# Kernel optimization log

Measured on AMD Instinct MI355X. Metric: run time of the kernel, lower is better.

Reference implementation:

```python
import jax, jax.numpy as jnp
import numpy as np
from jax import lax

# PRPN constants (match init_kwargs)
NSLOTS = 15
NLOOKBACK = 1
RESOLUTION = 0.1
NLAYERS = 2
H = 1024      # nhid == ninp
NTOKEN = 32000
T, B = 256, 64
INF = 1e8


def masked_softmax(x, mask):
    # PRPN blocks.softmax: exp-normalize then multiply by gate mask
    e = jnp.exp(x - jnp.max(x, axis=-1, keepdims=True))
    e = e * mask
    return e / (jnp.sum(e, axis=-1, keepdims=True) + 1e-8)


def setup_inputs() -> dict:
    key = jax.random.key(0)
    ks = jax.random.split(key, 16)
    s = 0.02
    return {
        'tokens': jax.random.randint(ks[0], (T, B), 0, NTOKEN),
        'emb_table': s * jax.random.normal(ks[1], (NTOKEN, H), jnp.float32),
        'conv1_w': s * jax.random.normal(ks[2], (H, H, NLOOKBACK + 1), jnp.float32),
        'conv1_b': jnp.zeros((H,), jnp.float32),
        'bn1_gamma': jnp.ones((H,), jnp.float32),
        'bn1_beta': jnp.zeros((H,), jnp.float32),
        'conv2_w': s * jax.random.normal(ks[3], (2, H // 2, 1), jnp.float32),
        'conv2_b': jnp.zeros((2,), jnp.float32),
        'reader_wih': s * jax.random.normal(ks[4], (NLAYERS, 4 * H, H), jnp.float32),
        'reader_whh': s * jax.random.normal(ks[5], (NLAYERS, 4 * H, H), jnp.float32),
        'reader_bih': jnp.zeros((NLAYERS, 4 * H), jnp.float32),
        'reader_bhh': jnp.zeros((NLAYERS, 4 * H), jnp.float32),
        'reader_summ_w': s * jax.random.normal(ks[6], (NLAYERS, H, 2 * H), jnp.float32),
        'reader_summ_b': jnp.zeros((NLAYERS, H), jnp.float32),
        'pred_summ_w': s * jax.random.normal(ks[7], (H, 2 * H), jnp.float32),
        'pred_summ_b': jnp.zeros((H,), jnp.float32),
        'ffd_w': s * jax.random.normal(ks[8], (H, 2 * H), jnp.float32),
        'ffd_b': jnp.zeros((H,), jnp.float32),
        'ffd_gamma': jnp.ones((H,), jnp.float32),
        'ffd_beta': jnp.zeros((H,), jnp.float32),
    }


def _parser_gates(emb, conv1_w, conv1_b, bn1_gamma, bn1_beta, conv2_w, conv2_b):
    # emb: (T, B, H). Parser state init: zeros lookback embs, +inf cum_gate.
    t = emb.shape[0]
    emb_last = jnp.concatenate([jnp.zeros((NLOOKBACK,) + emb.shape[1:], emb.dtype), emb], axis=0)
    x = jnp.transpose(emb_last, (1, 2, 0))  # (B, H, T+lookback)
    h = lax.conv_general_dilated(x, conv1_w, (1,), 'VALID',
                                 dimension_numbers=('NCH', 'OIH', 'NCH'))
    h = h + conv1_b[None, :, None]
    h = bn1_gamma[None, :, None] * h + bn1_beta[None, :, None]  # BatchNorm1d (eval, mean=0,var=1)
    h = jax.nn.relu(h)
    g = lax.conv_general_dilated(h, conv2_w, (1,), 'VALID', feature_group_count=2,
                                 dimension_numbers=('NCH', 'OIH', 'NCH'))
    g = jax.nn.sigmoid(g + conv2_b[None, :, None])  # (B, 2, T)
    gate, gate_next = g[:, 0], g[:, 1]  # (B, T)
    cum_gate = jnp.concatenate([jnp.full((gate.shape[0], NSLOTS), INF, gate.dtype), gate], axis=1)
    # gate_hat[:, t, j] = cum_gate[:, (NSLOTS - j) + t], slots stacked for i = NSLOTS..1
    idx = jnp.arange(t)[:, None] + (NSLOTS - jnp.arange(NSLOTS))[None, :]
    gate_hat = cum_gate[:, idx]  # (B, T, NSLOTS)
    mg = jnp.cumprod(jax.nn.sigmoid((gate[:, :, None] - gate_hat) / RESOLUTION * 10 + 5), axis=2)
    mgn = jnp.cumprod(jax.nn.sigmoid((gate_next[:, :, None] - gate_hat) / RESOLUTION * 10 + 5), axis=2)
    return mg, mgn  # (B, T, NSLOTS)


def _prpn_forward(tokens, emb_table, conv1_w, conv1_b, bn1_gamma, bn1_beta, conv2_w, conv2_b,
                  reader_wih, reader_whh, reader_bih, reader_bhh, reader_summ_w, reader_summ_b,
                  pred_summ_w, pred_summ_b, ffd_w, ffd_b, ffd_gamma, ffd_beta):
    t, b = tokens.shape
    emb = emb_table[tokens]  # (T, B, H)
    mg, mgn = _parser_gates(emb, conv1_w, conv1_b, bn1_gamma, bn1_beta, conv2_w, conv2_b)
    mg_t = jnp.transpose(mg, (1, 0, 2))   # (T, B, S)
    mgn_t = jnp.transpose(mgn, (1, 0, 2))
    inv_sqrt_h = 1.0 / np.sqrt(H).astype(np.float32)

    def step(carry, xs):
        rh, rc, pm = carry  # (L,B,S,H), (L,B,S,H), (B,S,H)
        emb_i, mg_i, mgn_i = xs
        h = emb_i
        new_rh, new_rc = [], []
        for j in range(NLAYERS):
            mh, mc = rh[j], rc[j]
            key = jnp.concatenate([h, mh[:, -1]], axis=1) @ reader_summ_w[j].T + reader_summ_b[j]
            logits = jnp.einsum('bsh,bh->bs', mh, key) * inv_sqrt_h
            att = masked_softmax(logits, mg_i)
            sel_h = jnp.einsum('bs,bsh->bh', att, mh)
            sel_c = jnp.einsum('bs,bsh->bh', att, mc)
            gates = h @ reader_wih[j].T + reader_bih[j] + sel_h @ reader_whh[j].T + reader_bhh[j]
            ig, fg, gg, og = jnp.split(gates, 4, axis=1)
            c_new = jax.nn.sigmoid(fg) * sel_c + jax.nn.sigmoid(ig) * jnp.tanh(gg)
            h = jax.nn.sigmoid(og) * jnp.tanh(c_new)
            new_rh.append(jnp.concatenate([mh[:, 1:], h[:, None]], axis=1))
            new_rc.append(jnp.concatenate([mc[:, 1:], c_new[:, None]], axis=1))
        # predictor attention over its own slot memory, gated by memory_gate_next
        key = jnp.concatenate([h, pm[:, -1]], axis=1) @ pred_summ_w.T + pred_summ_b
        logits = jnp.einsum('bsh,bh->bs', pm, key) * inv_sqrt_h
        att = masked_softmax(logits, mgn_i)
        sel = jnp.einsum('bs,bsh->bh', att, pm)
        pm = jnp.concatenate([pm[:, 1:], h[:, None]], axis=1)
        return (jnp.stack(new_rh), jnp.stack(new_rc), pm), (h, sel)

    z = jnp.zeros((NLAYERS, b, NSLOTS, H), emb.dtype)
    carry0 = (z, z, jnp.zeros((b, NSLOTS, H), emb.dtype))
    _, (hs, sels) = lax.scan(step, carry0, (emb, mg_t, mgn_t))
    x = jnp.concatenate([hs.reshape(-1, H), sels.reshape(-1, H)], axis=1)  # (T*B, 2H)
    out = jnp.tanh(ffd_gamma * (x @ ffd_w.T + ffd_b) + ffd_beta)  # PredictNetwork.ffd (BN eval)
    return out


def reference(tokens, emb_table, conv1_w, conv1_b, bn1_gamma, bn1_beta, conv2_w, conv2_b,
              reader_wih, reader_whh, reader_bih, reader_bhh, reader_summ_w, reader_summ_b,
              pred_summ_w, pred_summ_b, ffd_w, ffd_b, ffd_gamma, ffd_beta):
    out = _prpn_forward(tokens, emb_table, conv1_w, conv1_b, bn1_gamma, bn1_beta, conv2_w, conv2_b,
                        reader_wih, reader_whh, reader_bih, reader_bhh, reader_summ_w, reader_summ_b,
                        pred_summ_w, pred_summ_b, ffd_w, ffd_b, ffd_gamma, ffd_beta)
    mask = tokens != 0
    return out, mask
```

## Files before the change

kernel.cpp:

```cpp
#include <hip/hip_runtime.h>


typedef _Float16 half8 __attribute__((ext_vector_type(8)));
typedef float f32x4 __attribute__((ext_vector_type(4)));

#define LSTR 56

__device__ __forceinline__ float sigm(float x) { return 1.0f / (1.0f + expf(-x)); }

__device__ __forceinline__ void store_ct(float* p, float v)    { *p = v; }
__device__ __forceinline__ void store_ct(_Float16* p, float v) { *p = (_Float16)v; }

__device__ __forceinline__ void mfma_loop(const _Float16* __restrict__ Ag, int lda,
                                          const _Float16* __restrict__ Bg, int ldb,
                                          int K, _Float16* As, _Float16* Bs, f32x4* acc)
{
  const int tid = threadIdx.x;
  const int lr  = tid >> 2;
  const int lc  = (tid & 3) << 3;
  const int ln  = tid & 63;
  const int wv  = tid >> 6;
  const int m15 = ln & 15;
  const int q   = ln >> 4;
  const _Float16* ap = Ag + (size_t)lr * lda + lc;
  const _Float16* bp = Bg + (size_t)lr * ldb + lc;
  _Float16* asw = As + lr * LSTR + lc;
  _Float16* bsw = Bs + lr * LSTR + lc;
  const _Float16* asr = As + (wv * 16 + m15) * LSTR + q * 8;
  const _Float16* bsr = Bs + m15 * LSTR + q * 8;
  half8 av = *(const half8*)ap;
  half8 bv = *(const half8*)bp;
  for (int k0 = 0; k0 < K; k0 += 32) {
    __syncthreads();
    *(half8*)asw = av;
    *(half8*)bsw = bv;
    __syncthreads();
    if (k0 + 32 < K) {
      ap += 32; bp += 32;
      av = *(const half8*)ap;
      bv = *(const half8*)bp;
    }
    half8 a = *(const half8*)asr;
#pragma unroll
    for (int j = 0; j < 4; j++) {
      half8 b = *(const half8*)(bsr + j * 16 * LSTR);
      acc[j] = __builtin_amdgcn_mfma_f32_16x16x32_f16(a, b, acc[j], 0, 0, 0);
    }
  }
}

template <int ACT, typename CT>
__global__ __launch_bounds__(256) void gemm_bt(const _Float16* __restrict__ A, int lda,
                                               const _Float16* __restrict__ B, int ldb,
                                               CT* __restrict__ C, int ldc, int K,
                                               const float* __restrict__ p0,
                                               const float* __restrict__ p1,
                                               const float* __restrict__ p2)
{
  __shared__ __align__(16) _Float16 As[64 * LSTR];
  __shared__ __align__(16) _Float16 Bs[64 * LSTR];
  f32x4 acc[4] = {};
  const int ntile = blockIdx.x, mtile = blockIdx.y;
  mfma_loop(A + (size_t)mtile * 64 * lda, lda, B + (size_t)ntile * 64 * ldb, ldb, K, As, Bs, acc);
  const int ln = threadIdx.x & 63, wv = threadIdx.x >> 6;
  const int m15 = ln & 15, q = ln >> 4;
#pragma unroll
  for (int j = 0; j < 4; j++) {
    const int col = ntile * 64 + j * 16 + m15;
    float b0 = 0.f, b1 = 0.f, b2 = 0.f;
    if (ACT == 0) {
      if (p0) b0 = p0[col];
      if (p1) b0 += p1[col];
    } else {
      b0 = p0[col]; b1 = p1[col]; b2 = p2[col];
    }
#pragma unroll
    for (int r = 0; r < 4; r++) {
      const int row = mtile * 64 + wv * 16 + q * 4 + r;
      float v = acc[j][r];
      if (ACT == 0) v += b0;
      else {
        v = b0 * (v + b1) + b2;
        v = (ACT == 1) ? fmaxf(v, 0.f) : tanhf(v);
      }
      store_ct(&C[(size_t)row * ldc + col], v);
    }
  }
}

struct SegP { const _Float16* B; float* C; const float* b1; const float* b2; int ldb; int ldc; };

__device__ void bundle_tile(const _Float16* __restrict__ A, const SegP sg, int ntile,
                            _Float16* As, _Float16* Bs)
{
  f32x4 acc[4] = {};
  mfma_loop(A, 1024, sg.B + (size_t)ntile * 64 * sg.ldb, sg.ldb, 1024, As, Bs, acc);
  const int ln = threadIdx.x & 63, wv = threadIdx.x >> 6;
  const int m15 = ln & 15, q = ln >> 4;
#pragma unroll
  for (int j = 0; j < 4; j++) {
    const int col = ntile * 64 + j * 16 + m15;
    float bb = 0.f;
    if (sg.b1) bb += sg.b1[col];
    if (sg.b2) bb += sg.b2[col];
#pragma unroll
    for (int r = 0; r < 4; r++) {
      const int row = wv * 16 + q * 4 + r;
      sg.C[(size_t)row * sg.ldc + col] = acc[j][r] + bb;
    }
  }
}

template <typename KT, typename GT>
__device__ void cell_body(int b, int c0, int nch, int t,
    const KT* __restrict__ keyA, const float* __restrict__ keyB,
    const GT* __restrict__ gatesIn,
    const float* __restrict__ ringH, const float* __restrict__ ringC,
    const float* __restrict__ proj, const float* __restrict__ mask,
    float* __restrict__ hRingOut, float* __restrict__ cRingOut,
    _Float16* __restrict__ hHalf, float* s_key, float* s_att)
{
  const int tid = threadIdx.x;
  for (int i = tid; i < 1024; i += 256)
    s_key[i] = (float)keyA[b * 1024 + i] + keyB[b * 1024 + i];
  __syncthreads();
  const int wv = tid >> 6, ln = tid & 63;
  for (int s = wv; s < 15; s += 4) {
    const float* hr = ringH + ((size_t)((t + s) & 15) * 64 + b) * 1024;
    float p = 0.f;
    for (int i = ln; i < 1024; i += 64) p = fmaf(hr[i], s_key[i], p);
    for (int off = 32; off > 0; off >>= 1) p += __shfl_down(p, off, 64);
    if (ln == 0) s_att[s] = p * 0.03125f;
  }
  __syncthreads();
  if (tid == 0) {
    float mx = -1e30f;
    for (int s = 0; s < 15; s++) mx = fmaxf(mx, s_att[s]);
    float den = 1e-8f, e[15];
    for (int s = 0; s < 15; s++) { e[s] = expf(s_att[s] - mx) * mask[b * 15 + s]; den += e[s]; }
    float inv = 1.f / den;
    for (int s = 0; s < 15; s++) s_att[s] = e[s] * inv;
  }
  __syncthreads();
  float att[15];
  int poff[15], coff[15];
#pragma unroll
  for (int s = 0; s < 15; s++) {
    att[s] = s_att[s];
    const int phs = (t + s) & 15;
    poff[s] = phs * 262144 + b * 4096;
    coff[s] = phs * 65536 + b * 1024;
  }
  for (int c = c0 + tid; c < c0 + nch; c += 256) {
    float g[4];
#pragma unroll
    for (int gi = 0; gi < 4; gi++) {
      const int gidx = gi * 1024 + c;
      float a = (float)gatesIn[(size_t)b * 4096 + gidx];
      for (int s = 0; s < 15; s++) a = fmaf(att[s], proj[(size_t)poff[s] + gidx], a);
      g[gi] = a;
    }
    float selc = 0.f;
    for (int s = 0; s < 15; s++) selc = fmaf(att[s], ringC[(size_t)coff[s] + c], selc);
    const float ig = sigm(g[0]), fg = sigm(g[1]), gg = tanhf(g[2]), og = sigm(g[3]);
    const float cn = fg * selc + ig * gg;
    const float h  = og * tanhf(cn);
    cRingOut[b * 1024 + c] = cn;
    hRingOut[b * 1024 + c] = h;
    hHalf[b * 1024 + c]    = (_Float16)h;
  }
}

__device__ void pred_body(int b, int c0, int nch, int t,
    const float* __restrict__ keyA, const float* __restrict__ keyB,
    const float* __restrict__ ringH, const float* __restrict__ mask,
    _Float16* __restrict__ xrow, float* s_key, float* s_att)
{
  const int tid = threadIdx.x;
  for (int i = tid; i < 1024; i += 256)
    s_key[i] = keyA[b * 1024 + i] + keyB[b * 1024 + i];
  __syncthreads();
  const int wv = tid >> 6, ln = tid & 63;
  for (int s = wv; s < 15; s += 4) {
    const float* hr = ringH + ((size_t)((t + s) & 15) * 64 + b) * 1024;
    float p = 0.f;
    for (int i = ln; i < 1024; i += 64) p = fmaf(hr[i], s_key[i], p);
    for (int off = 32; off > 0; off >>= 1) p += __shfl_down(p, off, 64);
    if (ln == 0) s_att[s] = p * 0.03125f;
  }
  __syncthreads();
  if (tid == 0) {
    float mx = -1e30f;
    for (int s = 0; s < 15; s++) mx = fmaxf(mx, s_att[s]);
    float den = 1e-8f, e[15];
    for (int s = 0; s < 15; s++) { e[s] = expf(s_att[s] - mx) * mask[b * 15 + s]; den += e[s]; }
    float inv = 1.f / den;
    for (int s = 0; s < 15; s++) s_att[s] = e[s] * inv;
  }
  __syncthreads();
  float att[15];
  int hoff[15];
#pragma unroll
  for (int s = 0; s < 15; s++) { att[s] = s_att[s]; hoff[s] = ((t + s) & 15) * 65536 + b * 1024; }
  const float* hNew = ringH + (size_t)((t + 15) & 15) * 65536 + b * 1024;
  for (int c = c0 + tid; c < c0 + nch; c += 256) {
    float sel = 0.f;
    for (int s = 0; s < 15; s++) sel = fmaf(att[s], ringH[(size_t)hoff[s] + c], sel);
    const float h = hNew[c];
    xrow[(size_t)b * 2048 + c]        = (_Float16)h;
    xrow[(size_t)b * 2048 + 1024 + c] = (_Float16)sel;
  }
}

__device__ __forceinline__ void gsync(unsigned* arrive, unsigned* release, unsigned ph, int bid)
{
  __syncthreads();
  const int tid = threadIdx.x;
  if (bid == 0) {
    if (tid >= 1) {
      while (__hip_atomic_load(&arrive[tid << 5], __ATOMIC_RELAXED, __HIP_MEMORY_SCOPE_AGENT) < ph)
        __builtin_amdgcn_s_sleep(1);
    }
    __syncthreads();
    if (tid == 0) {
      __threadfence();
      __hip_atomic_store(release, ph, __ATOMIC_RELAXED, __HIP_MEMORY_SCOPE_AGENT);
    }
    __syncthreads();
  } else {
    if (tid == 0) {
      __threadfence();
      __hip_atomic_store(&arrive[bid << 5], ph, __ATOMIC_RELAXED, __HIP_MEMORY_SCOPE_AGENT);
      while (__hip_atomic_load(release, __ATOMIC_RELAXED, __HIP_MEMORY_SCOPE_AGENT) < ph)
        __builtin_amdgcn_s_sleep(1);
      __threadfence();
    }
    __syncthreads();
  }
}

struct ScanArgs {
  const _Float16 *embkey, *embgates, *wihF, *whhF, *wsmF, *wpdF;
  const float *mg, *mgn, *bih, *bhh, *bsm, *bpd;
  float *ringH0, *ringC0, *ringH1, *ringC1, *P0, *P1;
  float *kc0, *kc1, *kcp0, *kcp1, *key1s, *gates1i, *keypred;
  _Float16 *h0h, *h1h, *xbuf;
  unsigned *bar;
};

__global__ __launch_bounds__(256, 1) void k_scan(ScanArgs A)
{
  __shared__ __align__(16) _Float16 As[64 * LSTR];
  __shared__ __align__(16) _Float16 Bs[64 * LSTR];
  float* s_key = (float*)As;
  float* s_att = (float*)Bs;
  const int bid = blockIdx.x;
  unsigned* arrive  = A.bar;
  unsigned* release = A.bar + 8192;
  unsigned ph = 0;

  cell_body<_Float16, _Float16>(bid >> 2, (bid & 3) << 8, 256, 0,
      A.embkey, A.kc0, A.embgates, A.ringH0, A.ringC0, A.P0, A.mg,
      A.ringH0 + (size_t)15 * 65536, A.ringC0 + (size_t)15 * 65536, A.h0h, s_key, s_att);
  gsync(arrive, release, ++ph, bid);

  for (int t = 0; t < 256; ++t) {
    const int w15 = (t + 15) & 15;
    if (bid < 160) {
      SegP sg; int nt;
      if (bid < 64)       { sg = SegP{A.whhF,                 A.P0 + (size_t)w15 * 262144, nullptr,      nullptr,      1024, 4096}; nt = bid; }
      else if (bid < 80)  { sg = SegP{A.wsmF + 1024,          A.kc0,                       nullptr,      nullptr,      2048, 1024}; nt = bid - 64; }
      else if (bid < 144) { sg = SegP{A.wihF + 4194304,       A.gates1i,                   A.bih + 4096, A.bhh + 4096, 1024, 4096}; nt = bid - 80; }
      else                { sg = SegP{A.wsmF + 2097152,       A.key1s,                     A.bsm + 1024, nullptr,      2048, 1024}; nt = bid - 144; }
      bundle_tile(A.h0h, sg, nt, As, Bs);
    } else if (bid < 224 && t > 0) {
      pred_body(bid - 160, 0, 1024, t - 1, A.keypred, ((t - 1) & 1) ? A.kcp0 : A.kcp1,
                A.ringH1, A.mgn + (size_t)(t - 1) * 960, A.xbuf + (size_t)(t - 1) * 131072, s_key, s_att);
    }
    gsync(arrive, release, ++ph, bid);
    cell_body<float, float>(bid >> 2, (bid & 3) << 8, 256, t,
        A.key1s, A.kc1, A.gates1i, A.ringH1, A.ringC1, A.P1, A.mg + (size_t)t * 960,
        A.ringH1 + (size_t)w15 * 65536, A.ringC1 + (size_t)w15 * 65536, A.h1h, s_key, s_att);
    gsync(arrive, release, ++ph, bid);
    if (bid < 112) {
      SegP sg; int nt;
      float* kcpW = (t & 1) ? A.kcp1 : A.kcp0;
      if (bid < 64)       { sg = SegP{A.whhF + 4194304,        A.P1 + (size_t)w15 * 262144, nullptr, nullptr, 1024, 4096}; nt = bid; }
      else if (bid < 80)  { sg = SegP{A.wsmF + 2097152 + 1024, A.kc1,                       nullptr, nullptr, 2048, 1024}; nt = bid - 64; }
      else if (bid < 96)  { sg = SegP{A.wpdF,                  A.keypred,                   A.bpd,   nullptr, 2048, 1024}; nt = bid - 80; }
      else                { sg = SegP{A.wpdF + 1024,           kcpW,                        nullptr, nullptr, 2048, 1024}; nt = bid - 96; }
      bundle_tile(A.h1h, sg, nt, As, Bs);
    } else if (bid < 240 && t < 255) {
      const int bb = (bid - 112) >> 1, c0 = ((bid - 112) & 1) << 9;
      cell_body<_Float16, _Float16>(bb, c0, 512, t + 1,
          A.embkey + (size_t)(t + 1) * 65536, A.kc0, A.embgates + (size_t)(t + 1) * 262144,
          A.ringH0, A.ringC0, A.P0, A.mg + (size_t)(t + 1) * 960,
          A.ringH0 + (size_t)(t & 15) * 65536, A.ringC0 + (size_t)(t & 15) * 65536, A.h0h, s_key, s_att);
    }
    gsync(arrive, release, ++ph, bid);
  }
  pred_body(bid >> 2, (bid & 3) << 8, 256, 255, A.keypred, A.kcp0,
            A.ringH1, A.mgn + (size_t)255 * 960, A.xbuf + (size_t)255 * 131072, s_key, s_att);
}

__global__ void k_zero(float* __restrict__ p, int n) {
  int i = blockIdx.x * 256 + threadIdx.x;
  const int st = gridDim.x * 256;
  for (; i < n; i += st) p[i] = 0.f;
}

__global__ void k_cvt(const float* __restrict__ s, _Float16* __restrict__ d, int n) {
  int i = blockIdx.x * 256 + threadIdx.x;
  const int st = gridDim.x * 256;
  for (; i < n; i += st) d[i] = (_Float16)s[i];
}

__global__ void k_w1r(const float* __restrict__ w, _Float16* __restrict__ d) {
  const int i = blockIdx.x * 256 + threadIdx.x;
  if (i >= 2097152) return;
  const int o = i >> 11, kk = i & 2047;
  const int src = (kk < 1024) ? (o * 2048 + kk * 2) : (o * 2048 + (kk - 1024) * 2 + 1);
  d[i] = (_Float16)w[src];
}

__global__ void k_emb(const int* __restrict__ tokens, const float* __restrict__ table,
                      _Float16* __restrict__ embpair, float* __restrict__ maskOut)
{
  const int tb = blockIdx.x;
  const int t = tb >> 6, b = tb & 63;
  const int tok = tokens[tb];
  const float* row = table + (size_t)tok * 1024;
  _Float16* dst1 = embpair + (size_t)tb * 2048 + 1024;
  for (int i = threadIdx.x; i < 1024; i += 256) {
    const _Float16 v = (_Float16)row[i];
    dst1[i] = v;
    if (t + 1 < 256) embpair[(size_t)(tb + 64) * 2048 + i] = v;
    if (t == 0)      embpair[(size_t)b * 2048 + i] = (_Float16)0.f;
  }
  if (threadIdx.x == 0) maskOut[tb] = (tok != 0) ? 1.f : 0.f;
}

__global__ __launch_bounds__(128) void k_conv2(const _Float16* __restrict__ hcv,
                                               const float* __restrict__ w2, const float* __restrict__ b2,
                                               float* __restrict__ gate, float* __restrict__ gaten)
{
  const int r = blockIdx.x;
  const int wv = threadIdx.x >> 6, ln = threadIdx.x & 63;
  const _Float16* hr = hcv + (size_t)r * 1024 + wv * 512;
  const float* wr = w2 + wv * 512;
  float p = 0.f;
  for (int i = ln; i < 512; i += 64) p = fmaf((float)hr[i], wr[i], p);
  for (int off = 32; off > 0; off >>= 1) p += __shfl_down(p, off, 64);
  if (ln == 0) {
    const float v = sigm(p + b2[wv]);
    (wv ? gaten : gate)[r] = v;
  }
}

__global__ void k_masks(const float* __restrict__ gate, const float* __restrict__ gaten,
                        float* __restrict__ mg, float* __restrict__ mgn)
{
  const int i = blockIdx.x * 256 + threadIdx.x;
  if (i >= 16384) return;
  const int t = i >> 6, b = i & 63;
  const float gc = gate[i], gn = gaten[i];
  float p = 1.f, q = 1.f;
  for (int s = 0; s < 15; s++) {
    const float gh = (s <= t) ? gate[(t - s) * 64 + b] : 1e8f;
    p *= sigm((gc - gh) * 100.f + 5.f);
    q *= sigm((gn - gh) * 100.f + 5.f);
    mg[(size_t)i * 15 + s] = p;
    mgn[(size_t)i * 15 + s] = q;
  }
}

extern "C" void kernel_launch(void* const* d_in, const int* in_sizes, int n_in,
                              void* d_out, int out_size, void* d_ws, size_t ws_size,
                              hipStream_t stream)
{
  (void)in_sizes; (void)n_in; (void)out_size; (void)ws_size;
  const int*   tokens = (const int*)d_in[0];
  const float* table  = (const float*)d_in[1];
  const float* w1     = (const float*)d_in[2];
  const float* c1b    = (const float*)d_in[3];
  const float* g1     = (const float*)d_in[4];
  const float* bt1    = (const float*)d_in[5];
  const float* w2     = (const float*)d_in[6];
  const float* c2b    = (const float*)d_in[7];
  const float* wih    = (const float*)d_in[8];
  const float* whh    = (const float*)d_in[9];
  const float* bih    = (const float*)d_in[10];
  const float* bhh    = (const float*)d_in[11];
  const float* wsm    = (const float*)d_in[12];
  const float* bsm    = (const float*)d_in[13];
  const float* wpd    = (const float*)d_in[14];
  const float* bpd    = (const float*)d_in[15];
  const float* ffw    = (const float*)d_in[16];
  const float* ffb    = (const float*)d_in[17];
  const float* ffg    = (const float*)d_in[18];
  const float* ffbt   = (const float*)d_in[19];

  float* outp    = (float*)d_out;
  float* maskOut = outp + 16777216;

  char* wp_ = (char*)d_ws;
  auto alloc = [&](size_t b) { void* r = (void*)wp_; wp_ += (b + 255) & ~(size_t)255; return r; };

  _Float16* embpair  = (_Float16*)alloc(67108864);
  _Float16* hcv      = (_Float16*)alloc(33554432);
  _Float16* embgates = (_Float16*)alloc(134217728);
  _Float16* wihF     = (_Float16*)alloc(16777216);
  _Float16* whhF     = (_Float16*)alloc(16777216);
  _Float16* wsmF     = (_Float16*)alloc(8388608);
  _Float16* wpdF     = (_Float16*)alloc(4194304);
  _Float16* ffwF     = (_Float16*)alloc(4194304);
  _Float16* w1rF     = (_Float16*)alloc(4194304);
  _Float16* h0h      = (_Float16*)alloc(131072);
  _Float16* h1h      = (_Float16*)alloc(131072);
  float* gate    = (float*)alloc(65536);
  float* gaten   = (float*)alloc(65536);
  float* mg      = (float*)alloc(983040);
  float* mgn     = (float*)alloc(983040);
  float* key1s   = (float*)alloc(262144);
  float* gates1i = (float*)alloc(1048576);
  float* keypred = (float*)alloc(262144);
  float* zb = (float*)alloc(51413120);
  float* ringH0 = zb;
  float* ringC0 = ringH0 + 1048576;
  float* ringH1 = ringC0 + 1048576;
  float* ringC1 = ringH1 + 1048576;
  float* P0     = ringC1 + 1048576;
  float* P1     = P0 + 4194304;
  float* kc0    = P1 + 4194304;
  float* kc1    = kc0 + 65536;
  float* kcp0   = kc1 + 65536;
  float* kcp1   = kcp0 + 65536;
  unsigned* bar = (unsigned*)(kcp1 + 65536);

  _Float16* xbuf   = embpair;
  _Float16* embkey = hcv;

  k_zero<<<4096, 256, 0, stream>>>(zb, 12853280);
  k_emb<<<16384, 256, 0, stream>>>(tokens, table, embpair, maskOut);
  k_cvt<<<8192, 256, 0, stream>>>(wih, wihF, 8388608);
  k_cvt<<<8192, 256, 0, stream>>>(whh, whhF, 8388608);
  k_cvt<<<8192, 256, 0, stream>>>(wsm, wsmF, 4194304);
  k_cvt<<<4096, 256, 0, stream>>>(wpd, wpdF, 2097152);
  k_cvt<<<4096, 256, 0, stream>>>(ffw, ffwF, 2097152);
  k_w1r<<<8192, 256, 0, stream>>>(w1, w1rF);
  gemm_bt<1, _Float16><<<dim3(16, 256), 256, 0, stream>>>(embpair, 2048, w1rF, 2048, hcv, 1024, 2048, g1, c1b, bt1);
  k_conv2<<<16384, 128, 0, stream>>>(hcv, w2, c2b, gate, gaten);
  k_masks<<<64, 256, 0, stream>>>(gate, gaten, mg, mgn);
  gemm_bt<0, _Float16><<<dim3(64, 256), 256, 0, stream>>>(embpair + 1024, 2048, wihF, 1024, embgates, 4096, 1024, bih, bhh, nullptr);
  gemm_bt<0, _Float16><<<dim3(16, 256), 256, 0, stream>>>(embpair + 1024, 2048, wsmF, 2048, embkey, 1024, 1024, bsm, nullptr, nullptr);

  ScanArgs sa;
  sa.embkey = embkey; sa.embgates = embgates;
  sa.wihF = wihF; sa.whhF = whhF; sa.wsmF = wsmF; sa.wpdF = wpdF;
  sa.mg = mg; sa.mgn = mgn; sa.bih = bih; sa.bhh = bhh; sa.bsm = bsm; sa.bpd = bpd;
  sa.ringH0 = ringH0; sa.ringC0 = ringC0; sa.ringH1 = ringH1; sa.ringC1 = ringC1;
  sa.P0 = P0; sa.P1 = P1;
  sa.kc0 = kc0; sa.kc1 = kc1; sa.kcp0 = kcp0; sa.kcp1 = kcp1;
  sa.key1s = key1s; sa.gates1i = gates1i; sa.keypred = keypred;
  sa.h0h = h0h; sa.h1h = h1h; sa.xbuf = xbuf;
  sa.bar = bar;
  k_scan<<<dim3(256), dim3(256), 0, stream>>>(sa);

  gemm_bt<2, float><<<dim3(16, 256), 256, 0, stream>>>(xbuf, 2048, ffwF, 2048, outp, 1024, 2048, ffg, ffb, ffbt);
}
```

Measured before the change: 29.07 ms.

## Keep per-block weight tiles resident in LDS across persistent scan steps

Each persistent block now loads its 64-row weight slice (up to 128KB fp16) into shared memory once before the time loop and reuses it for every recurrent GEMM tile, instead of restreaming weights from global memory each step. Work assignment is reshuffled so blocks 160-255 own the layer-1 GEMM tiles with resident weights, while a new streamed path (register-prefetched, double-buffered LDS) handles the kcp tiles and the layer-0 cell work moves to other blocks. This removes repeated weight traffic per timestep, at the cost of a very large LDS footprint and high register use for the prefetch arrays.

New measurement: 30.72 ms. 1.06x slower.

```diff
diff --git a/kernel.cpp b/kernel.cpp
--- a/kernel.cpp
+++ b/kernel.cpp
@@ -5,6 +5,8 @@
 typedef float f32x4 __attribute__((ext_vector_type(4)));
 
 #define LSTR 56
+#define WSTR 1028
+#define ASTR 36
 
 __device__ __forceinline__ float sigm(float x) { return 1.0f / (1.0f + expf(-x)); }
 
@@ -88,25 +90,90 @@
   }
 }
 
-struct SegP { const _Float16* B; float* C; const float* b1; const float* b2; int ldb; int ldc; };
-
-__device__ void bundle_tile(const _Float16* __restrict__ A, const SegP sg, int ntile,
-                            _Float16* As, _Float16* Bs)
-{
-  f32x4 acc[4] = {};
-  mfma_loop(A, 1024, sg.B + (size_t)ntile * 64 * sg.ldb, sg.ldb, 1024, As, Bs, acc);
+__device__ __forceinline__ void mfma_resident(const _Float16* __restrict__ Ag,
+                                              const _Float16* __restrict__ W,
+                                              _Float16 (*Asd)[64 * ASTR], f32x4* acc)
+{
+  const int tid = threadIdx.x;
+  const int r = tid >> 2, c0 = (tid & 3) << 3;
+  const int ln = tid & 63, wv = tid >> 6, m15 = ln & 15, q = ln >> 4;
+  const _Float16* ap = Ag + (size_t)r * 1024 + c0;
+  half8 av[32];
+#pragma unroll
+  for (int k = 0; k < 32; ++k) av[k] = *(const half8*)(ap + k * 32);
+  const int awoff = r * ASTR + c0;
+  const int aroff = (wv * 16 + m15) * ASTR + q * 8;
+  const _Float16* wr = W + m15 * WSTR + q * 8;
+  *(half8*)(Asd[0] + awoff) = av[0];
+#pragma unroll
+  for (int k = 0; k < 32; ++k) {
+    __syncthreads();
+    if (k + 1 < 32) *(half8*)(Asd[(k + 1) & 1] + awoff) = av[k + 1];
+    half8 a = *(const half8*)(Asd[k & 1] + aroff);
+#pragma unroll
+    for (int j = 0; j < 4; j++) {
+      half8 b = *(const half8*)(wr + j * 16 * WSTR + k * 32);
+      acc[j] = __builtin_amdgcn_mfma_f32_16x16x32_f16(a, b, acc[j], 0, 0, 0);
+    }
+  }
+}
+
+__device__ __forceinline__ void mfma_streamed(const _Float16* __restrict__ Ag,
+                                              const _Float16* __restrict__ Bg, int ldb,
+                                              _Float16 (*Asd)[64 * ASTR],
+                                              _Float16 (*Bsd)[64 * ASTR], f32x4* acc)
+{
+  const int tid = threadIdx.x;
+  const int r = tid >> 2, c0 = (tid & 3) << 3;
+  const int ln = tid & 63, wv = tid >> 6, m15 = ln & 15, q = ln >> 4;
+  const _Float16* ap = Ag + (size_t)r * 1024 + c0;
+  const _Float16* bp = Bg + (size_t)r * ldb + c0;
+  half8 av[32], bv[32];
+#pragma unroll
+  for (int k = 0; k < 16; ++k) {
+    av[k] = *(const half8*)(ap + k * 32);
+    bv[k] = *(const half8*)(bp + k * 32);
+  }
+  const int awoff = r * ASTR + c0;
+  const int aroff = (wv * 16 + m15) * ASTR + q * 8;
+  const int broff = m15 * ASTR + q * 8;
+  *(half8*)(Asd[0] + awoff) = av[0];
+  *(half8*)(Bsd[0] + awoff) = bv[0];
+#pragma unroll
+  for (int k = 0; k < 32; ++k) {
+    if (k < 16) {
+      av[k + 16] = *(const half8*)(ap + (k + 16) * 32);
+      bv[k + 16] = *(const half8*)(bp + (k + 16) * 32);
+    }
+    __syncthreads();
+    if (k + 1 < 32) {
+      *(half8*)(Asd[(k + 1) & 1] + awoff) = av[k + 1];
+      *(half8*)(Bsd[(k + 1) & 1] + awoff) = bv[k + 1];
+    }
+    half8 a = *(const half8*)(Asd[k & 1] + aroff);
+#pragma unroll
+    for (int j = 0; j < 4; j++) {
+      half8 b = *(const half8*)(Bsd[k & 1] + broff + j * 16 * ASTR);
+      acc[j] = __builtin_amdgcn_mfma_f32_16x16x32_f16(a, b, acc[j], 0, 0, 0);
+    }
+  }
+}
+
+__device__ __forceinline__ void store_tile(float* __restrict__ C, int ldc, int nt,
+                                           const float* b1, const float* b2, f32x4* acc)
+{
   const int ln = threadIdx.x & 63, wv = threadIdx.x >> 6;
   const int m15 = ln & 15, q = ln >> 4;
 #pragma unroll
   for (int j = 0; j < 4; j++) {
-    const int col = ntile * 64 + j * 16 + m15;
+    const int col = nt * 64 + j * 16 + m15;
     float bb = 0.f;
-    if (sg.b1) bb += sg.b1[col];
-    if (sg.b2) bb += sg.b2[col];
+    if (b1) bb += b1[col];
+    if (b2) bb += b2[col];
 #pragma unroll
     for (int r = 0; r < 4; r++) {
       const int row = wv * 16 + q * 4 + r;
-      sg.C[(size_t)row * sg.ldc + col] = acc[j][r] + bb;
+      C[(size_t)row * ldc + col] = acc[j][r] + bb;
     }
   }
 }
@@ -250,15 +317,30 @@
 
 __global__ __launch_bounds__(256, 1) void k_scan(ScanArgs A)
 {
-  __shared__ __align__(16) _Float16 As[64 * LSTR];
-  __shared__ __align__(16) _Float16 Bs[64 * LSTR];
-  float* s_key = (float*)As;
-  float* s_att = (float*)Bs;
+  __shared__ __align__(16) _Float16 Wlds[64 * WSTR];
+  __shared__ __align__(16) _Float16 Asd[2][64 * ASTR];
+  __shared__ __align__(16) _Float16 Bsd[2][64 * ASTR];
+  float* s_key = (float*)Bsd;
+  float* s_att = (float*)Bsd + 1024;
   const int bid = blockIdx.x;
   unsigned* arrive  = A.bar;
   unsigned* release = A.bar + 8192;
   unsigned ph = 0;
 
+  {
+    const _Float16* src; int ldb;
+    if (bid < 64)       { src = A.whhF                  + (size_t)bid         * 65536;  ldb = 1024; }
+    else if (bid < 80)  { src = A.wsmF + 1024           + (size_t)(bid - 64)  * 131072; ldb = 2048; }
+    else if (bid < 144) { src = A.wihF + 4194304        + (size_t)(bid - 80)  * 65536;  ldb = 1024; }
+    else if (bid < 160) { src = A.wsmF + 2097152        + (size_t)(bid - 144) * 131072; ldb = 2048; }
+    else if (bid < 224) { src = A.whhF + 4194304        + (size_t)(bid - 160) * 65536;  ldb = 1024; }
+    else if (bid < 240) { src = A.wsmF + 2097152 + 1024 + (size_t)(bid - 224) * 131072; ldb = 2048; }
+    else                { src = A.wpdF                  + (size_t)(bid - 240) * 131072; ldb = 2048; }
+    const int r = threadIdx.x >> 2, c0 = (threadIdx.x & 3) << 3;
+    for (int it = 0; it < 32; ++it)
+      *(half8*)(Wlds + r * WSTR + c0 + it * 32) = *(const half8*)(src + (size_t)r * ldb + c0 + it * 32);
+  }
+
   cell_body<_Float16, _Float16>(bid >> 2, (bid & 3) << 8, 256, 0,
       A.embkey, A.kc0, A.embgates, A.ringH0, A.ringC0, A.P0, A.mg,
       A.ringH0 + (size_t)15 * 65536, A.ringC0 + (size_t)15 * 65536, A.h0h, s_key, s_att);
@@ -267,12 +349,14 @@
   for (int t = 0; t < 256; ++t) {
     const int w15 = (t + 15) & 15;
     if (bid < 160) {
-      SegP sg; int nt;
-      if (bid < 64)       { sg = SegP{A.whhF,                 A.P0 + (size_t)w15 * 262144, nullptr,      nullptr,      1024, 4096}; nt = bid; }
-      else if (bid < 80)  { sg = SegP{A.wsmF + 1024,          A.kc0,                       nullptr,      nullptr,      2048, 1024}; nt = bid - 64; }
-      else if (bid < 144) { sg = SegP{A.wihF + 4194304,       A.gates1i,                   A.bih + 4096, A.bhh + 4096, 1024, 4096}; nt = bid - 80; }
-      else                { sg = SegP{A.wsmF + 2097152,       A.key1s,                     A.bsm + 1024, nullptr,      2048, 1024}; nt = bid - 144; }
-      bundle_tile(A.h0h, sg, nt, As, Bs);
+      float* C; const float* b1 = nullptr; const float* b2 = nullptr; int ldc; int nt;
+      if (bid < 64)       { C = A.P0 + (size_t)w15 * 262144; ldc = 4096; nt = bid; }
+      else if (bid < 80)  { C = A.kc0;     ldc = 1024; nt = bid - 64; }
+      else if (bid < 144) { C = A.gates1i; ldc = 4096; b1 = A.bih + 4096; b2 = A.bhh + 4096; nt = bid - 80; }
+      else                { C = A.key1s;   ldc = 1024; b1 = A.bsm + 1024; nt = bid - 144; }
+      f32x4 acc[4] = {};
+      mfma_resident(A.h0h, Wlds, Asd, acc);
+      store_tile(C, ldc, nt, b1, b2, acc);
     } else if (bid < 224 && t > 0) {
       pred_body(bid - 160, 0, 1024, t - 1, A.keypred, ((t - 1) & 1) ? A.kcp0 : A.kcp1,
                 A.ringH1, A.mgn + (size_t)(t - 1) * 960, A.xbuf + (size_t)(t - 1) * 131072, s_key, s_att);
@@ -282,16 +366,21 @@
         A.key1s, A.kc1, A.gates1i, A.ringH1, A.ringC1, A.P1, A.mg + (size_t)t * 960,
         A.ringH1 + (size_t)w15 * 65536, A.ringC1 + (size_t)w15 * 65536, A.h1h, s_key, s_att);
     gsync(arrive, release, ++ph, bid);
-    if (bid < 112) {
-      SegP sg; int nt;
+    if (bid >= 160) {
+      float* C; const float* b1 = nullptr; int ldc; int nt;
+      if (bid < 224)      { C = A.P1 + (size_t)w15 * 262144; ldc = 4096; nt = bid - 160; }
+      else if (bid < 240) { C = A.kc1;     ldc = 1024; nt = bid - 224; }
+      else                { C = A.keypred; ldc = 1024; b1 = A.bpd; nt = bid - 240; }
+      f32x4 acc[4] = {};
+      mfma_resident(A.h1h, Wlds, Asd, acc);
+      store_tile(C, ldc, nt, b1, nullptr, acc);
+    } else if (bid < 16) {
       float* kcpW = (t & 1) ? A.kcp1 : A.kcp0;
-      if (bid < 64)       { sg = SegP{A.whhF + 4194304,        A.P1 + (size_t)w15 * 262144, nullptr, nullptr, 1024, 4096}; nt = bid; }
-      else if (bid < 80)  { sg = SegP{A.wsmF + 2097152 + 1024, A.kc1,                       nullptr, nullptr, 2048, 1024}; nt = bid - 64; }
-      else if (bid < 96)  { sg = SegP{A.wpdF,                  A.keypred,                   A.bpd,   nullptr, 2048, 1024}; nt = bid - 80; }
-      else                { sg = SegP{A.wpdF + 1024,           kcpW,                        nullptr, nullptr, 2048, 1024}; nt = bid - 96; }
-      bundle_tile(A.h1h, sg, nt, As, Bs);
-    } else if (bid < 240 && t < 255) {
-      const int bb = (bid - 112) >> 1, c0 = ((bid - 112) & 1) << 9;
+      f32x4 acc[4] = {};
+      mfma_streamed(A.h1h, A.wpdF + 1024 + (size_t)bid * 131072, 2048, Asd, Bsd, acc);
+      store_tile(kcpW, 1024, bid, nullptr, nullptr, acc);
+    } else if (bid < 144 && t < 255) {
+      const int bb = (bid - 16) >> 1, c0 = ((bid - 16) & 1) << 9;
       cell_body<_Float16, _Float16>(bb, c0, 512, t + 1,
           A.embkey + (size_t)(t + 1) * 65536, A.kc0, A.embgates + (size_t)(t + 1) * 262144,
           A.ringH0, A.ringC0, A.P0, A.mg + (size_t)(t + 1) * 960,
```
